# Performance work log

Measured on AMD Instinct MI355X. Metric: run time of the kernel, lower is better.

## Reference

```python
import jax, jax.numpy as jnp
import numpy as np

N = 50000      # nodes
E = 800000     # edges (before self-loops)
IN = 256       # in_channels
HID = 128      # hidden_channels
OUT = 128      # out_channels
NEG_SLOPE = 0.2
EPS = 1e-16


def setup_inputs() -> dict:
    key = jax.random.key(0)
    ks = jax.random.split(key, 16)
    p = lambda k, shape: jax.random.normal(k, shape, jnp.float32) * 0.1
    return {
        "x": jax.random.normal(ks[0], (N, IN), jnp.float32),
        "edge_index": jax.random.randint(ks[1], (2, E), 0, N, dtype=jnp.int64),
        # semantic MLP
        "W1": p(ks[2], (IN, HID)), "b1": jnp.zeros((HID,), jnp.float32),
        "W2": p(ks[3], (HID, HID)), "b2": jnp.zeros((HID,), jnp.float32),
        # gat1: HID -> HID//2, heads=4, concat -> 2*HID
        "g1_W": p(ks[4], (HID, 4 * (HID // 2))),
        "g1_as": p(ks[5], (4, HID // 2)), "g1_ad": p(ks[6], (4, HID // 2)),
        "g1_b": jnp.zeros((4 * (HID // 2),), jnp.float32),
        # gat2: 2*HID -> OUT, heads=2, mean -> OUT
        "g2_W": p(ks[7], (2 * HID, 2 * OUT)),
        "g2_as": p(ks[8], (2, OUT)), "g2_ad": p(ks[9], (2, OUT)),
        "g2_b": jnp.zeros((OUT,), jnp.float32),
        # gat3: OUT -> OUT, heads=1, mean -> OUT
        "g3_W": p(ks[10], (OUT, OUT)),
        "g3_as": p(ks[11], (1, OUT)), "g3_ad": p(ks[12], (1, OUT)),
        "g3_b": jnp.zeros((OUT,), jnp.float32),
    }


def _gat(h_in, src, dst, W, a_src, a_dst, bias, heads, concat, n):
    # Linear projection into heads: [n, H, C]
    h = (h_in @ W).reshape(n, heads, -1)
    alpha_s = jnp.sum(h * a_src[None], axis=-1)  # [n, H]
    alpha_d = jnp.sum(h * a_dst[None], axis=-1)  # [n, H]
    e = jax.nn.leaky_relu(alpha_s[src] + alpha_d[dst], NEG_SLOPE)  # [E', H]
    # segment softmax over edges grouped by destination node
    m = jax.ops.segment_max(e, dst, num_segments=n)
    ex = jnp.exp(e - m[dst])
    denom = jax.ops.segment_sum(ex, dst, num_segments=n)
    alpha = ex / (denom[dst] + EPS)  # [E', H]
    msg = h[src] * alpha[..., None]  # [E', H, C]
    out = jax.ops.segment_sum(msg, dst, num_segments=n)  # [n, H, C]
    out = out.reshape(n, -1) if concat else out.mean(axis=1)
    return out + bias


def reference(x, edge_index, W1, b1, W2, b2,
              g1_W, g1_as, g1_ad, g1_b,
              g2_W, g2_as, g2_ad, g2_b,
              g3_W, g3_as, g3_ad, g3_b):
    n = x.shape[0]
    # PyG GATConv add_self_loops=True: append self-loop edges once
    loops = jnp.arange(n, dtype=edge_index.dtype)
    src = jnp.concatenate([edge_index[0], loops])
    dst = jnp.concatenate([edge_index[1], loops])
    # semantic MLP (inference: dropout = identity)
    h = jax.nn.relu(x @ W1 + b1)
    h = jax.nn.relu(h @ W2 + b2)
    h = jax.nn.elu(_gat(h, src, dst, g1_W, g1_as, g1_ad, g1_b, 4, True, n))
    h = jax.nn.elu(_gat(h, src, dst, g2_W, g2_as, g2_ad, g2_b, 2, False, n))
    h = _gat(h, src, dst, g3_W, g3_as, g3_ad, g3_b, 1, False, n)
    return h
```

## Files before the change

### kernel.cpp

```cpp
#include <hip/hip_runtime.h>
#include <math.h>


#define NEG_SLOPE 0.2f
#define EPS_DEN 1e-16f

typedef __attribute__((ext_vector_type(8))) short short8;
typedef __attribute__((ext_vector_type(4))) float f32x4;
typedef __attribute__((ext_vector_type(2))) float f32x2;
typedef __attribute__((ext_vector_type(4))) unsigned short u16x4;

__device__ inline unsigned short f2b(float f) {
  unsigned u = __builtin_bit_cast(unsigned, f);
  unsigned r = (u + 0x7fffu + ((u >> 16) & 1u)) >> 16;
  return (unsigned short)r;
}
__device__ inline float b2f(unsigned short u) {
  return __builtin_bit_cast(float, (unsigned)u << 16);
}

__device__ inline void glds16(const void* g, void* l) {
  __builtin_amdgcn_global_load_lds(
      (const __attribute__((address_space(1))) void*)g,
      (__attribute__((address_space(3))) void*)l, 16, 0, 0);
}

__device__ inline f32x2 pk_fma(f32x2 a, f32x2 b, f32x2 c) {
  f32x2 d;
  asm("v_pk_fma_f32 %0, %1, %2, %3" : "=v"(d) : "v"(a), "v"(b), "v"(c));
  return d;
}

__device__ inline void accum8(f32x2 acc2[4], const short8 r, float w) {
  const f32x2 wv = {w, w};
  const unsigned* u = (const unsigned*)&r;
#pragma unroll
  for (int p = 0; p < 4; p++) {
    const unsigned lo = u[p] << 16;
    const unsigned hi = u[p] & 0xffff0000u;
    f32x2 val = {__builtin_bit_cast(float, lo), __builtin_bit_cast(float, hi)};
    acc2[p] = pk_fma(val, wv, acc2[p]);
  }
}

template <int H>
__device__ inline void loadH(const float* p, float* v) {
  if constexpr (H == 4) {
    float4 t = *(const float4*)p;
    v[0] = t.x; v[1] = t.y; v[2] = t.z; v[3] = t.w;
  } else if constexpr (H == 2) {
    float2 t = *(const float2*)p;
    v[0] = t.x; v[1] = t.y;
  } else {
    v[0] = *p;
  }
}

template <int ACT, int OBF, int H, int CC>
__global__ __launch_bounds__(256) void mfma_gemm(
    const unsigned short* __restrict__ A, const unsigned short* __restrict__ Bt,
    const float* __restrict__ bias, float* __restrict__ Cf,
    unsigned short* __restrict__ Cb, const float* __restrict__ a_s,
    const float* __restrict__ a_d, float* __restrict__ alS,
    float* __restrict__ alD, int n, int K, int M) {
  __shared__ unsigned short As[128 * 64];
  __shared__ unsigned short Bs[128 * 64];

  const int tid = threadIdx.x;
  const int w = tid >> 6, lane = tid & 63;
  const int row0 = blockIdx.x * 128, col0 = blockIdx.y * 128;
  const int lr = lane >> 3, lg = lane & 7;
  const int lm = lane & 15, kg = lane >> 4;
  const int wm = (w >> 1) * 64, wn = (w & 1) * 64;

  f32x4 acc[4][4];
#pragma unroll
  for (int i = 0; i < 4; i++)
#pragma unroll
    for (int j = 0; j < 4; j++) acc[i][j] = {0.f, 0.f, 0.f, 0.f};

  const int swz = (lg ^ lr) << 3;

  for (int k0 = 0; k0 < K; k0 += 64) {
    __syncthreads();
#pragma unroll
    for (int it = 0; it < 4; it++) {
      const int r = w * 32 + it * 8;
      glds16(A + (size_t)(row0 + r + lr) * K + k0 + swz, &As[r * 64]);
      glds16(Bt + (size_t)(col0 + r + lr) * K + k0 + swz, &Bs[r * 64]);
    }
    __syncthreads();

#pragma unroll
    for (int kh = 0; kh < 2; kh++) {
      const int sw = ((kh * 4 + kg) ^ (lm & 7)) << 3;
      short8 aF[4], bF[4];
#pragma unroll
      for (int i = 0; i < 4; i++) {
        aF[i] = *(const short8*)&As[(wm + i * 16 + lm) * 64 + sw];
        bF[i] = *(const short8*)&Bs[(wn + i * 16 + lm) * 64 + sw];
      }
#pragma unroll
      for (int i = 0; i < 4; i++)
#pragma unroll
        for (int j = 0; j < 4; j++)
          acc[i][j] = __builtin_amdgcn_mfma_f32_16x16x32_bf16(
              aF[i], bF[j], acc[i][j], 0, 0, 0);
    }
  }

  const int r4 = kg * 4;

  if constexpr (H > 0) {
    const int head = (col0 + wn) / CC;
    const int ch0 = (col0 + wn) % CC;
    float asv[4], adv[4];
#pragma unroll
    for (int j = 0; j < 4; j++) {
      asv[j] = a_s[head * CC + ch0 + j * 16 + lm];
      adv[j] = a_d[head * CC + ch0 + j * 16 + lm];
    }
    float psA[4][4], pdA[4][4];
#pragma unroll
    for (int i = 0; i < 4; i++) {
#pragma unroll
      for (int r = 0; r < 4; r++) {
        float ps = 0.f, pd = 0.f;
#pragma unroll
        for (int j = 0; j < 4; j++) {
          ps += acc[i][j][r] * asv[j];
          pd += acc[i][j][r] * adv[j];
        }
#pragma unroll
        for (int off = 1; off < 16; off <<= 1) {
          ps += __shfl_xor(ps, off, 64);
          pd += __shfl_xor(pd, off, 64);
        }
        psA[i][r] = ps;
        pdA[i][r] = pd;
      }
    }
    if constexpr (CC == 64) {
      if (lm == 0) {
#pragma unroll
        for (int i = 0; i < 4; i++)
#pragma unroll
          for (int r = 0; r < 4; r++) {
            const int row = row0 + wm + i * 16 + r4 + r;
            if (row < n) {
              alS[(size_t)row * H + head] = psA[i][r];
              alD[(size_t)row * H + head] = pdA[i][r];
            }
          }
      }
    } else {
      __shared__ float redS[4][64];
      __shared__ float redD[4][64];
      if (lm == 0) {
#pragma unroll
        for (int i = 0; i < 4; i++)
#pragma unroll
          for (int r = 0; r < 4; r++) {
            redS[w][i * 16 + r4 + r] = psA[i][r];
            redD[w][i * 16 + r4 + r] = pdA[i][r];
          }
      }
      __syncthreads();
      if ((w & 1) == 0) {
        const int row = row0 + wm + lane;
        if (row < n) {
          const int hd = col0 / CC;
          alS[(size_t)row * H + hd] = redS[w][lane] + redS[w + 1][lane];
          alD[(size_t)row * H + hd] = redD[w][lane] + redD[w + 1][lane];
        }
      }
    }
  }

#pragma unroll
  for (int j = 0; j < 4; j++) {
    const int col = col0 + wn + j * 16 + lm;
    const float bv = bias ? bias[col] : 0.f;
#pragma unroll
    for (int i = 0; i < 4; i++) {
#pragma unroll
      for (int r = 0; r < 4; r++) {
        const int row = row0 + wm + i * 16 + r4 + r;
        if (row < n) {
          float v = acc[i][j][r] + bv;
          if (ACT == 1) v = v > 0.f ? v : 0.f;
          if (OBF)
            Cb[(size_t)row * M + col] = f2b(v);
          else
            Cf[(size_t)row * M + col] = v;
        }
      }
    }
  }
}

__global__ __launch_bounds__(256) void mlp_fused_kernel(
    const unsigned short* __restrict__ X, const unsigned short* __restrict__ W1t,
    const float* __restrict__ b1, const unsigned short* __restrict__ W2t,
    const float* __restrict__ b2, unsigned short* __restrict__ H2, int n) {
  __shared__ unsigned short As[128 * 64];
  __shared__ unsigned short Bs[128 * 64];
  __shared__ unsigned short H1s[128 * 136];

  const int tid = threadIdx.x;
  const int w = tid >> 6, lane = tid & 63;
  const int row0 = blockIdx.x * 128;
  const int lr = lane >> 3, lg = lane & 7;
  const int lm = lane & 15, kg = lane >> 4;
  const int wm = (w >> 1) * 64, wn = (w & 1) * 64;
  const int swz = (lg ^ lr) << 3;
  const int r4 = kg * 4;

  f32x4 acc[4][4];
#pragma unroll
  for (int i = 0; i < 4; i++)
#pragma unroll
    for (int j = 0; j < 4; j++) acc[i][j] = {0.f, 0.f, 0.f, 0.f};

  for (int k0 = 0; k0 < 256; k0 += 64) {
    __syncthreads();
#pragma unroll
    for (int it = 0; it < 4; it++) {
      const int r = w * 32 + it * 8;
      glds16(X + (size_t)(row0 + r + lr) * 256 + k0 + swz, &As[r * 64]);
      glds16(W1t + (size_t)(r + lr) * 256 + k0 + swz, &Bs[r * 64]);
    }
    __syncthreads();
#pragma unroll
    for (int kh = 0; kh < 2; kh++) {
      const int sw = ((kh * 4 + kg) ^ (lm & 7)) << 3;
      short8 aF[4], bF[4];
#pragma unroll
      for (int i = 0; i < 4; i++) {
        aF[i] = *(const short8*)&As[(wm + i * 16 + lm) * 64 + sw];
        bF[i] = *(const short8*)&Bs[(wn + i * 16 + lm) * 64 + sw];
      }
#pragma unroll
      for (int i = 0; i < 4; i++)
#pragma unroll
        for (int j = 0; j < 4; j++)
          acc[i][j] = __builtin_amdgcn_mfma_f32_16x16x32_bf16(
              aF[i], bF[j], acc[i][j], 0, 0, 0);
    }
  }

#pragma unroll
  for (int j = 0; j < 4; j++) {
    const int col = wn + j * 16 + lm;
    const float bv = b1[col];
#pragma unroll
    for (int i = 0; i < 4; i++) {
#pragma unroll
      for (int r = 0; r < 4; r++) {
        const int lrow = wm + i * 16 + r4 + r;
        float v = acc[i][j][r] + bv;
        v = v > 0.f ? v : 0.f;
        H1s[lrow * 136 + col] = f2b(v);
      }
    }
  }
#pragma unroll
  for (int i = 0; i < 4; i++)
#pragma unroll
    for (int j = 0; j < 4; j++) acc[i][j] = {0.f, 0.f, 0.f, 0.f};
  __syncthreads();

  for (int k0 = 0; k0 < 128; k0 += 64) {
    __syncthreads();
#pragma unroll
    for (int it = 0; it < 4; it++) {
      const int r = w * 32 + it * 8;
      glds16(W2t + (size_t)(r + lr) * 128 + k0 + swz, &Bs[r * 64]);
    }
    __syncthreads();
#pragma unroll
    for (int kh = 0; kh < 2; kh++) {
      const int swB = ((kh * 4 + kg) ^ (lm & 7)) << 3;
      const int kofs = k0 + (kh * 4 + kg) * 8;
      short8 aF[4], bF[4];
#pragma unroll
      for (int i = 0; i < 4; i++) {
        aF[i] = *(const short8*)&H1s[(wm + i * 16 + lm) * 136 + kofs];
        bF[i] = *(const short8*)&Bs[(wn + i * 16 + lm) * 64 + swB];
      }
#pragma unroll
      for (int i = 0; i < 4; i++)
#pragma unroll
        for (int j = 0; j < 4; j++)
          acc[i][j] = __builtin_amdgcn_mfma_f32_16x16x32_bf16(
              aF[i], bF[j], acc[i][j], 0, 0, 0);
    }
  }

#pragma unroll
  for (int j = 0; j < 4; j++) {
    const int col = wn + j * 16 + lm;
    const float bv = b2[col];
#pragma unroll
    for (int i = 0; i < 4; i++) {
#pragma unroll
      for (int r = 0; r < 4; r++) {
        const int row = row0 + wm + i * 16 + r4 + r;
        if (row < n) {
          float v = acc[i][j][r] + bv;
          v = v > 0.f ? v : 0.f;
          H2[(size_t)row * 128 + col] = f2b(v);
        }
      }
    }
  }
}

struct PrepArgs {
  const float* x; unsigned short* xb; long long nx;
  const float* W[5]; unsigned short* Wt[5];
  int K[5], M[5], t0[6];
  int* deg; int N;
};

__global__ __launch_bounds__(256) void fused_prep_kernel(PrepArgs a) {
  const int tid = threadIdx.x, bid = blockIdx.x, nb = gridDim.x;
  const long long gt = (long long)bid * 256 + tid;
  const long long gsz = (long long)nb * 256;
  __shared__ float tt[32][33];

  for (long long i = gt; i < a.N; i += gsz) a.deg[i] = 0;
  for (long long i = gt * 4; i < a.nx; i += gsz * 4) {
    float4 v = *(const float4*)(a.x + i);
    u16x4 u = {f2b(v.x), f2b(v.y), f2b(v.z), f2b(v.w)};
    *(u16x4*)(a.xb + i) = u;
  }
  for (int t = bid; t < a.t0[5]; t += nb) {
    int di = 0;
    while (t >= a.t0[di + 1]) di++;
    const int local = t - a.t0[di];
    const int K = a.K[di], M = a.M[di], mtiles = M / 32;
    const int mb = (local % mtiles) * 32, kb = (local / mtiles) * 32;
    const float* W = a.W[di];
    unsigned short* Wt = a.Wt[di];
    const int tx = tid & 31, ty = tid >> 5;
    __syncthreads();
#pragma unroll
    for (int i = 0; i < 4; i++)
      tt[ty + i * 8][tx] = W[(size_t)(kb + ty + i * 8) * M + mb + tx];
    __syncthreads();
#pragma unroll
    for (int i = 0; i < 4; i++)
      Wt[(size_t)(mb + ty + i * 8) * K + kb + tx] = f2b(tt[tx][ty + i * 8]);
  }
}

__global__ void count_rank_kernel(const int* __restrict__ edst,
                                  int* __restrict__ deg,
                                  int* __restrict__ rank, int E, int n) {
  int i = blockIdx.x * blockDim.x + threadIdx.x;
  if (i >= E + n) return;
  int d = (i < E) ? __builtin_nontemporal_load(edst + i) : (i - E);
  if ((unsigned)d < (unsigned)n) rank[i] = atomicAdd(&deg[d], 1);
}

__global__ __launch_bounds__(256) void block_reduce_kernel(
    const int* __restrict__ deg, int* __restrict__ bsum, int n) {
  __shared__ int s[256];
  const int t = threadIdx.x, i = blockIdx.x * 256 + t;
  s[t] = (i < n) ? deg[i] : 0;
  __syncthreads();
#pragma unroll
  for (int off = 128; off; off >>= 1) {
    if (t < off) s[t] += s[t + off];
    __syncthreads();
  }
  if (t == 0) bsum[blockIdx.x] = s[0];
}

__global__ __launch_bounds__(256) void scan_bsums_kernel(int* __restrict__ bsum,
                                                         int nb) {
  __shared__ int s[256];
  const int t = threadIdx.x;
  const int v = (t < nb) ? bsum[t] : 0;
  s[t] = v;
  __syncthreads();
#pragma unroll
  for (int off = 1; off < 256; off <<= 1) {
    int a = (t >= off) ? s[t - off] : 0;
    __syncthreads();
    s[t] += a;
    __syncthreads();
  }
  if (t < nb) bsum[t] = s[t] - v;
}

__global__ __launch_bounds__(256) void scan_final_kernel(
    const int* __restrict__ deg, const int* __restrict__ bsumx,
    int* __restrict__ rowptr, int n) {
  __shared__ int s[256];
  const int t = threadIdx.x, i = blockIdx.x * 256 + t;
  const int v = (i < n) ? deg[i] : 0;
  s[t] = v;
  __syncthreads();
#pragma unroll
  for (int off = 1; off < 256; off <<= 1) {
    int a = (t >= off) ? s[t - off] : 0;
    __syncthreads();
    s[t] += a;
    __syncthreads();
  }
  if (i < n) {
    const int base = bsumx[blockIdx.x];
    rowptr[i] = base + s[t] - v;
    if (i == n - 1) rowptr[n] = base + s[t];
  }
}

__global__ void scatter_kernel(const int* __restrict__ esrc,
                               const int* __restrict__ edst,
                               const int* __restrict__ rank,
                               const int* __restrict__ rowptr,
                               int* __restrict__ csr_src, int E, int n) {
  int i = blockIdx.x * blockDim.x + threadIdx.x;
  int tot = E + n;
  if (i >= tot) return;
  int s, d;
  if (i < E) {
    s = __builtin_nontemporal_load(esrc + i);
    d = __builtin_nontemporal_load(edst + i);
  } else {
    s = d = i - E;
  }
  if ((unsigned)d >= (unsigned)n || (unsigned)s >= (unsigned)n) return;
  int pos = rowptr[d] + __builtin_nontemporal_load(rank + i);
  csr_src[pos] = s;
}

template <int H, int C, bool CONCAT, int ACT, int OBF>
__global__ __launch_bounds__(256) void gat_fused_kernel(
    const unsigned short* __restrict__ proj, const float* __restrict__ alpha_s,
    const float* __restrict__ alpha_d, const int* __restrict__ rowptr,
    const int* __restrict__ csr_src, const float* __restrict__ bias,
    void* __restrict__ out, int n) {
  constexpr int HC = H * C;
  constexpr int ROWSPAN = HC / 8;
  constexpr int EDGES = 64 / ROWSPAN;
  constexpr int WLANES = C / 8;

  __shared__ float exs[4][64 * H];
  __shared__ int sids[4][64];

  const int wv = threadIdx.x >> 6;
  const int wid = (blockIdx.x * blockDim.x + threadIdx.x) >> 6;
  const int lane = threadIdx.x & 63;
  if (wid >= n) return;
  const int dst = wid;
  const int eslot = lane / ROWSPAN;
  const int sl = lane % ROWSPAN;
  const int h_lane = (sl * 8) / C;
  float* myex = &exs[wv][0];
  int* mysid = &sids[wv][0];

  float adv[H];
  loadH<H>(alpha_d + (size_t)dst * H, adv);
  const int rs = rowptr[dst], re = rowptr[dst + 1];

  float denomp[H];
#pragma unroll
  for (int h = 0; h < H; h++) denomp[h] = 0.f;
  f32x2 acc2[4];
#pragma unroll
  for (int p = 0; p < 4; p++) acc2[p] = {0.f, 0.f};

  const unsigned short* prow = proj + sl * 8;

  for (int base = rs; base < re; base += 64) {
    const int cnt = min(64, re - base);
    if (lane < cnt) {
      const int s = __builtin_nontemporal_load(csr_src + base + lane);
      mysid[lane] = s;
      float as[H];
      loadH<H>(alpha_s + (size_t)s * H, as);
#pragma unroll
      for (int h = 0; h < H; h++) {
        float e = as[h] + adv[h];
        e = e > 0.f ? e : NEG_SLOPE * e;
        const float ex = __expf(e);
        denomp[h] += ex;
        myex[lane * H + h] = ex;
      }
    }
    __builtin_amdgcn_wave_barrier();
    int j = eslot;
    for (; j + EDGES < cnt; j += 2 * EDGES) {
      const int s0 = mysid[j];
      const int s1 = mysid[j + EDGES];
      const float w0 = myex[j * H + h_lane];
      const float w1 = myex[(j + EDGES) * H + h_lane];
      const short8 r0 = *(const short8*)(prow + (size_t)s0 * HC);
      const short8 r1 = *(const short8*)(prow + (size_t)s1 * HC);
      accum8(acc2, r0, w0);
      accum8(acc2, r1, w1);
    }
    for (; j < cnt; j += EDGES) {
      const int s0 = mysid[j];
      const float w0 = myex[j * H + h_lane];
      const short8 r0 = *(const short8*)(prow + (size_t)s0 * HC);
      accum8(acc2, r0, w0);
    }
    __builtin_amdgcn_wave_barrier();
  }

  float acc[8];
#pragma unroll
  for (int p = 0; p < 4; p++) {
    acc[2 * p] = acc2[p].x;
    acc[2 * p + 1] = acc2[p].y;
  }

#pragma unroll
  for (int off = 32; off; off >>= 1)
#pragma unroll
    for (int h = 0; h < H; h++)
      denomp[h] += __shfl_xor(denomp[h], off, 64);
#pragma unroll
  for (int off = ROWSPAN; off < 64; off <<= 1)
#pragma unroll
    for (int k = 0; k < 8; k++) acc[k] += __shfl_xor(acc[k], off, 64);

  const float inv = 1.f / (denomp[h_lane] + EPS_DEN);
  float v[8];
#pragma unroll
  for (int k = 0; k < 8; k++) v[k] = acc[k] * inv;

  if (!CONCAT && H == 2) {
#pragma unroll
    for (int k = 0; k < 8; k++) v[k] += __shfl_xor(v[k], 16, 64);
  }

  if (CONCAT) {
    if (eslot != 0) return;
    const int c0 = sl * 8;
    float vv[8];
#pragma unroll
    for (int k = 0; k < 8; k++) {
      float t = v[k] + bias[c0 + k];
      if (ACT == 1) t = t > 0.f ? t : (__expf(t) - 1.f);
      vv[k] = t;
    }
    if (OBF) {
      short8 o;
#pragma unroll
      for (int k = 0; k < 8; k++) o[k] = (short)f2b(vv[k]);
      __builtin_nontemporal_store(
          o, (short8*)((unsigned short*)out + (size_t)dst * HC + c0));
    } else {
      float* op = (float*)out + (size_t)dst * HC + c0;
      f32x4 o0 = {vv[0], vv[1], vv[2], vv[3]};
      f32x4 o1 = {vv[4], vv[5], vv[6], vv[7]};
      __builtin_nontemporal_store(o0, (f32x4*)op);
      __builtin_nontemporal_store(o1, (f32x4*)(op + 4));
    }
  } else {
    if (eslot != 0 || sl >= WLANES) return;
    const int c0 = sl * 8;
    const float invH = 1.f / (float)H;
    float vv[8];
#pragma unroll
    for (int k = 0; k < 8; k++) {
      float t = v[k] * invH + bias[c0 + k];
      if (ACT == 1) t = t > 0.f ? t : (__expf(t) - 1.f);
      vv[k] = t;
    }
    if (OBF) {
      short8 o;
#pragma unroll
      for (int k = 0; k < 8; k++) o[k] = (short)f2b(vv[k]);
      __builtin_nontemporal_store(
          o, (short8*)((unsigned short*)out + (size_t)dst * C + c0));
    } else {
      float* op = (float*)out + (size_t)dst * C + c0;
      f32x4 o0 = {vv[0], vv[1], vv[2], vv[3]};
      f32x4 o1 = {vv[4], vv[5], vv[6], vv[7]};
      __builtin_nontemporal_store(o0, (f32x4*)op);
      __builtin_nontemporal_store(o1, (f32x4*)(op + 4));
    }
  }
}

extern "C" void kernel_launch(void* const* d_in, const int* in_sizes, int n_in,
                              void* d_out, int out_size, void* d_ws,
                              size_t ws_size, hipStream_t stream) {
  const float* x    = (const float*)d_in[0];
  const int*   ei   = (const int*)d_in[1];
  const float* W1   = (const float*)d_in[2];
  const float* b1   = (const float*)d_in[3];
  const float* W2   = (const float*)d_in[4];
  const float* b2   = (const float*)d_in[5];
  const float* g1W  = (const float*)d_in[6];
  const float* g1as = (const float*)d_in[7];
  const float* g1ad = (const float*)d_in[8];
  const float* g1b  = (const float*)d_in[9];
  const float* g2W  = (const float*)d_in[10];
  const float* g2as = (const float*)d_in[11];
  const float* g2ad = (const float*)d_in[12];
  const float* g2b  = (const float*)d_in[13];
  const float* g3W  = (const float*)d_in[14];
  const float* g3as = (const float*)d_in[15];
  const float* g3ad = (const float*)d_in[16];
  const float* g3b  = (const float*)d_in[17];

  const int N = in_sizes[0] / 256;
  const int E = in_sizes[1] / 2;
  const int Etot = E + N;
  const int NT = (N + 127) / 128;
  const int NP = NT * 128;
  const int NB = (N + 255) / 256;

  char* p = (char*)d_ws;
  unsigned short* Pb  = (unsigned short*)p; p += (size_t)NP * 256 * 2;
  unsigned short* xb  = (unsigned short*)p; p += (size_t)NP * 256 * 2;
  unsigned short* h2b = (unsigned short*)p; p += (size_t)NP * 128 * 2;
  unsigned short* W1t = (unsigned short*)p; p += (size_t)128 * 256 * 2;
  unsigned short* W2t = (unsigned short*)p; p += (size_t)128 * 128 * 2;
  unsigned short* g1Wt = (unsigned short*)p; p += (size_t)256 * 128 * 2;
  unsigned short* g2Wt = (unsigned short*)p; p += (size_t)256 * 256 * 2;
  unsigned short* g3Wt = (unsigned short*)p; p += (size_t)128 * 128 * 2;
  float* alB = (float*)p; p += (size_t)N * 14 * 4;
  float* alS1 = alB;
  float* alD1 = alB + (size_t)4 * N;
  float* alS2 = alB + (size_t)8 * N;
  float* alD2 = alB + (size_t)10 * N;
  float* alS3 = alB + (size_t)12 * N;
  float* alD3 = alB + (size_t)13 * N;
  int* deg    = (int*)p; p += (size_t)N * 4;
  int* rowptr = (int*)p; p += (size_t)(N + 1) * 4;
  int* bsum   = (int*)p; p += 256 * 4;
  int* rank   = (int*)p; p += (size_t)Etot * 4;
  int* csrsrc = (int*)p;

  const int* esrc = ei;
  const int* edst = ei + E;
  unsigned short* act1b = xb;
  unsigned short* act2b = h2b;

  PrepArgs pa;
  pa.x = x; pa.xb = xb; pa.nx = (long long)N * 256;
  pa.W[0] = W1;  pa.Wt[0] = W1t;  pa.K[0] = 256; pa.M[0] = 128;
  pa.W[1] = W2;  pa.Wt[1] = W2t;  pa.K[1] = 128; pa.M[1] = 128;
  pa.W[2] = g1W; pa.Wt[2] = g1Wt; pa.K[2] = 128; pa.M[2] = 256;
  pa.W[3] = g2W; pa.Wt[3] = g2Wt; pa.K[3] = 256; pa.M[3] = 256;
  pa.W[4] = g3W; pa.Wt[4] = g3Wt; pa.K[4] = 128; pa.M[4] = 128;
  pa.t0[0] = 0;
  for (int i = 0; i < 5; i++)
    pa.t0[i + 1] = pa.t0[i] + (pa.K[i] / 32) * (pa.M[i] / 32);
  pa.deg = deg; pa.N = N;
  fused_prep_kernel<<<512, 256, 0, stream>>>(pa);

  count_rank_kernel<<<(Etot + 255) / 256, 256, 0, stream>>>(edst, deg, rank, E,
                                                            N);
  block_reduce_kernel<<<NB, 256, 0, stream>>>(deg, bsum, N);
  scan_bsums_kernel<<<1, 256, 0, stream>>>(bsum, NB);
  scan_final_kernel<<<NB, 256, 0, stream>>>(deg, bsum, rowptr, N);
  scatter_kernel<<<(Etot + 255) / 256, 256, 0, stream>>>(esrc, edst, rank,
                                                         rowptr, csrsrc, E, N);

  mlp_fused_kernel<<<NT, 256, 0, stream>>>(xb, W1t, b1, W2t, b2, h2b, N);

  mfma_gemm<0, 1, 4, 64><<<dim3(NT, 2), 256, 0, stream>>>(
      h2b, g1Wt, nullptr, nullptr, Pb, g1as, g1ad, alS1, alD1, N, 128, 256);
  gat_fused_kernel<4, 64, true, 1, 1><<<(N + 3) / 4, 256, 0, stream>>>(
      Pb, alS1, alD1, rowptr, csrsrc, g1b, act1b, N);

  mfma_gemm<0, 1, 2, 128><<<dim3(NT, 2), 256, 0, stream>>>(
      act1b, g2Wt, nullptr, nullptr, Pb, g2as, g2ad, alS2, alD2, N, 256, 256);
  gat_fused_kernel<2, 128, false, 1, 1><<<(N + 3) / 4, 256, 0, stream>>>(
      Pb, alS2, alD2, rowptr, csrsrc, g2b, act2b, N);

  mfma_gemm<0, 1, 1, 128><<<dim3(NT, 1), 256, 0, stream>>>(
      act2b, g3Wt, nullptr, nullptr, Pb, g3as, g3ad, alS3, alD3, N, 128, 128);
  gat_fused_kernel<1, 128, false, 0, 0><<<(N + 3) / 4, 256, 0, stream>>>(
      Pb, alS3, alD3, rowptr, csrsrc, g3b, d_out, N);
}
```

Before: 457.9 us.

## Fuse GAT1 projection into MLP kernel and merge degree counting into prep

Measured after the change: 449.1 us. Within noise of the previous version (-1.9%).

```diff
diff --git a/kernel.cpp b/kernel.cpp
--- a/kernel.cpp
+++ b/kernel.cpp
@@ -199,10 +199,13 @@
   }
 }
 
-__global__ __launch_bounds__(256) void mlp_fused_kernel(
+__global__ __launch_bounds__(256) void mlp_g1_kernel(
     const unsigned short* __restrict__ X, const unsigned short* __restrict__ W1t,
     const float* __restrict__ b1, const unsigned short* __restrict__ W2t,
-    const float* __restrict__ b2, unsigned short* __restrict__ H2, int n) {
+    const float* __restrict__ b2, const unsigned short* __restrict__ G1Wt,
+    const float* __restrict__ a_s, const float* __restrict__ a_d,
+    float* __restrict__ alS, float* __restrict__ alD,
+    unsigned short* __restrict__ Pb, int n) {
   __shared__ unsigned short As[128 * 64];
   __shared__ unsigned short Bs[128 * 64];
   __shared__ unsigned short H1s[128 * 136];
@@ -297,6 +300,7 @@
     }
   }
 
+  __syncthreads();
 #pragma unroll
   for (int j = 0; j < 4; j++) {
     const int col = wn + j * 16 + lm;
@@ -305,11 +309,92 @@
     for (int i = 0; i < 4; i++) {
 #pragma unroll
       for (int r = 0; r < 4; r++) {
-        const int row = row0 + wm + i * 16 + r4 + r;
-        if (row < n) {
-          float v = acc[i][j][r] + bv;
-          v = v > 0.f ? v : 0.f;
-          H2[(size_t)row * 128 + col] = f2b(v);
+        const int lrow = wm + i * 16 + r4 + r;
+        float v = acc[i][j][r] + bv;
+        v = v > 0.f ? v : 0.f;
+        H1s[lrow * 136 + col] = f2b(v);
+      }
+    }
+  }
+  __syncthreads();
+
+  for (int c = 0; c < 2; c++) {
+#pragma unroll
+    for (int i = 0; i < 4; i++)
+#pragma unroll
+      for (int j = 0; j < 4; j++) acc[i][j] = {0.f, 0.f, 0.f, 0.f};
+
+    for (int k0 = 0; k0 < 128; k0 += 64) {
+      __syncthreads();
+#pragma unroll
+      for (int it = 0; it < 4; it++) {
+        const int r = w * 32 + it * 8;
+        glds16(G1Wt + (size_t)(c * 128 + r + lr) * 128 + k0 + swz,
+               &Bs[r * 64]);
+      }
+      __syncthreads();
+#pragma unroll
+      for (int kh = 0; kh < 2; kh++) {
+        const int swB = ((kh * 4 + kg) ^ (lm & 7)) << 3;
+        const int kofs = k0 + (kh * 4 + kg) * 8;
+        short8 aF[4], bF[4];
+#pragma unroll
+        for (int i = 0; i < 4; i++) {
+          aF[i] = *(const short8*)&H1s[(wm + i * 16 + lm) * 136 + kofs];
+          bF[i] = *(const short8*)&Bs[(wn + i * 16 + lm) * 64 + swB];
+        }
+#pragma unroll
+        for (int i = 0; i < 4; i++)
+#pragma unroll
+          for (int j = 0; j < 4; j++)
+            acc[i][j] = __builtin_amdgcn_mfma_f32_16x16x32_bf16(
+                aF[i], bF[j], acc[i][j], 0, 0, 0);
+      }
+    }
+
+    {
+      const int head = c * 2 + (wn >> 6);
+      float asv[4], adv[4];
+#pragma unroll
+      for (int j = 0; j < 4; j++) {
+        asv[j] = a_s[head * 64 + j * 16 + lm];
+        adv[j] = a_d[head * 64 + j * 16 + lm];
+      }
+#pragma unroll
+      for (int i = 0; i < 4; i++) {
+#pragma unroll
+        for (int r = 0; r < 4; r++) {
+          float ps = 0.f, pd = 0.f;
+#pragma unroll
+          for (int j = 0; j < 4; j++) {
+            ps += acc[i][j][r] * asv[j];
+            pd += acc[i][j][r] * adv[j];
+          }
+#pragma unroll
+          for (int off = 1; off < 16; off <<= 1) {
+            ps += __shfl_xor(ps, off, 64);
+            pd += __shfl_xor(pd, off, 64);
+          }
+          if (lm == 0) {
+            const int row = row0 + wm + i * 16 + r4 + r;
+            if (row < n) {
+              alS[(size_t)row * 4 + head] = ps;
+              alD[(size_t)row * 4 + head] = pd;
+            }
+          }
+        }
+      }
+    }
+
+#pragma unroll
+    for (int j = 0; j < 4; j++) {
+      const int col = c * 128 + wn + j * 16 + lm;
+#pragma unroll
+      for (int i = 0; i < 4; i++) {
+#pragma unroll
+        for (int r = 0; r < 4; r++) {
+          const int row = row0 + wm + i * 16 + r4 + r;
+          if (row < n) Pb[(size_t)row * 256 + col] = f2b(acc[i][j][r]);
         }
       }
     }
@@ -320,7 +405,7 @@
   const float* x; unsigned short* xb; long long nx;
   const float* W[5]; unsigned short* Wt[5];
   int K[5], M[5], t0[6];
-  int* deg; int N;
+  int* deg; int* rank; const int* edst; int E; int N;
 };
 
 __global__ __launch_bounds__(256) void fused_prep_kernel(PrepArgs a) {
@@ -329,7 +414,13 @@
   const long long gsz = (long long)nb * 256;
   __shared__ float tt[32][33];
 
-  for (long long i = gt; i < a.N; i += gsz) a.deg[i] = 0;
+  const long long etot = (long long)a.E + a.N;
+  for (long long i = gt; i < etot; i += gsz) {
+    int d = (i < a.E) ? __builtin_nontemporal_load(a.edst + i)
+                      : (int)(i - a.E);
+    if ((unsigned)d < (unsigned)a.N)
+      a.rank[i] = atomicAdd(&a.deg[d], 1);
+  }
   for (long long i = gt * 4; i < a.nx; i += gsz * 4) {
     float4 v = *(const float4*)(a.x + i);
     u16x4 u = {f2b(v.x), f2b(v.y), f2b(v.z), f2b(v.w)};
@@ -353,15 +444,6 @@
     for (int i = 0; i < 4; i++)
       Wt[(size_t)(mb + ty + i * 8) * K + kb + tx] = f2b(tt[tx][ty + i * 8]);
   }
-}
-
-__global__ void count_rank_kernel(const int* __restrict__ edst,
-                                  int* __restrict__ deg,
-                                  int* __restrict__ rank, int E, int n) {
-  int i = blockIdx.x * blockDim.x + threadIdx.x;
-  if (i >= E + n) return;
-  int d = (i < E) ? __builtin_nontemporal_load(edst + i) : (i - E);
-  if ((unsigned)d < (unsigned)n) rank[i] = atomicAdd(&deg[d], 1);
 }
 
 __global__ __launch_bounds__(256) void block_reduce_kernel(
@@ -645,6 +727,8 @@
   unsigned short* act1b = xb;
   unsigned short* act2b = h2b;
 
+  hipMemsetAsync(deg, 0, (size_t)N * 4, stream);
+
   PrepArgs pa;
   pa.x = x; pa.xb = xb; pa.nx = (long long)N * 256;
   pa.W[0] = W1;  pa.Wt[0] = W1t;  pa.K[0] = 256; pa.M[0] = 128;
@@ -655,21 +739,18 @@
   pa.t0[0] = 0;
   for (int i = 0; i < 5; i++)
     pa.t0[i + 1] = pa.t0[i] + (pa.K[i] / 32) * (pa.M[i] / 32);
-  pa.deg = deg; pa.N = N;
+  pa.deg = deg; pa.rank = rank; pa.edst = edst; pa.E = E; pa.N = N;
   fused_prep_kernel<<<512, 256, 0, stream>>>(pa);
 
-  count_rank_kernel<<<(Etot + 255) / 256, 256, 0, stream>>>(edst, deg, rank, E,
-                                                            N);
   block_reduce_kernel<<<NB, 256, 0, stream>>>(deg, bsum, N);
   scan_bsums_kernel<<<1, 256, 0, stream>>>(bsum, NB);
   scan_final_kernel<<<NB, 256, 0, stream>>>(deg, bsum, rowptr, N);
   scatter_kernel<<<(Etot + 255) / 256, 256, 0, stream>>>(esrc, edst, rank,
                                                          rowptr, csrsrc, E, N);
 
-  mlp_fused_kernel<<<NT, 256, 0, stream>>>(xb, W1t, b1, W2t, b2, h2b, N);
-
-  mfma_gemm<0, 1, 4, 64><<<dim3(NT, 2), 256, 0, stream>>>(
-      h2b, g1Wt, nullptr, nullptr, Pb, g1as, g1ad, alS1, alD1, N, 128, 256);
+  mlp_g1_kernel<<<NT, 256, 0, stream>>>(xb, W1t, b1, W2t, b2, g1Wt, g1as,
+                                        g1ad, alS1, alD1, Pb, N);
+
   gat_fused_kernel<4, 64, true, 1, 1><<<(N + 3) / 4, 256, 0, stream>>>(
       Pb, alS1, alD1, rowptr, csrsrc, g1b, act1b, N);
 
```
